# Optimization experiments

Hardware: AMD Instinct MI355X
Metric: run time of the kernel (lower is better)

Reference implementation:

```python
import jax, jax.numpy as jnp
import numpy as np
from jax import lax

DN = ('NCHW', 'OIHW', 'NCHW')


def conv3x3(x, w, b):
    y = lax.conv_general_dilated(x, w, (1, 1), [(1, 1), (1, 1)], dimension_numbers=DN)
    return y + b[None, :, None, None]


def lrelu(x, s):
    return jnp.where(x >= 0, x, s * x)


def layernorm_c(x, g, b, eps=1e-5):
    # LayerNorm over embed_dim; tokens are (h,w), so normalize the channel axis
    m = jnp.mean(x, axis=1, keepdims=True)
    v = jnp.var(x, axis=1, keepdims=True)
    return (x - m) / jnp.sqrt(v + eps) * g[None, :, None, None] + b[None, :, None, None]


def bilateral_corr(x1, x2, md):
    # bilateral cost volume on L2-normalized features:
    # out[b,d,h,w] = <x1n[b,:,h-dy,w-dx], x2n[b,:,h+dy,w+dx]>, (dy,dx) in [-md,md]^2
    def l2n(x):
        return x / jnp.maximum(jnp.linalg.norm(x, axis=1, keepdims=True), 1e-12)
    x1n, x2n = l2n(x1), l2n(x2)
    B, C, H, W = x1.shape
    p1 = jnp.pad(x1n, ((0, 0), (0, 0), (md, md), (md, md)))
    p2 = jnp.pad(x2n, ((0, 0), (0, 0), (md, md), (md, md)))
    outs = []
    for dy in range(-md, md + 1):
        for dx in range(-md, md + 1):
            a = p1[:, :, md - dy:md - dy + H, md - dx:md - dx + W]
            b = p2[:, :, md + dy:md + dy + H, md + dx:md + dx + W]
            outs.append(jnp.sum(a * b, axis=1))
    return jnp.stack(outs, axis=1)  # [B, (2md+1)^2, H, W]


def tail(xt, bi, gln, bln, w0, b0, wr1, br1, wr2, br2, w2, b2, w3, b3, wdec, bdec, wf, bf):
    xt = layernorm_c(xt, gln, bln)
    y = conv3x3(jnp.concatenate([xt, bi], axis=1), w0, b0)
    # resblock(64,64): lrelu(conv2(lrelu(conv1(y))) + y), slope 0.1
    s = y
    r = lrelu(conv3x3(y, wr1, br1), 0.1)
    r = conv3x3(r, wr2, br2) + s
    y = lrelu(r, 0.1)
    y = lrelu(conv3x3(y, w2, b2), 0.2)
    y = lrelu(conv3x3(y, w3, b3), 0.2)
    # ConvTranspose2d(64,64,3,stride=2,pad=1,out_pad=1): lhs-dilated conv with flipped kernel
    wd = jnp.transpose(jnp.flip(wdec, (-2, -1)), (1, 0, 2, 3))  # torch [in,out,kh,kw] -> OIHW
    y = lax.conv_general_dilated(y, wd, (1, 1), [(1, 2), (1, 2)], lhs_dilation=(2, 2), dimension_numbers=DN) + bdec[None, :, None, None]
    flow = conv3x3(y, wf, bf)  # [B, 2, 2H, 2W]
    B, _, H2, W2 = flow.shape
    # F.interpolate(scale_factor=4, mode='bilinear', align_corners=False) * 4
    return jax.image.resize(flow, (B, 2, 4 * H2, 4 * W2), method='bilinear') * 4.0


def setup_inputs():
    key = jax.random.key(0)
    ks = jax.random.split(key, 16)
    B, C, H, W = 4, 256, 96, 160
    md = 3
    r = lambda k, s, sc=0.05: jax.random.normal(k, s, jnp.float32) * sc
    return {
        'x1': jax.random.normal(ks[0], (B, C, H, W), jnp.float32),
        'x2': jax.random.normal(ks[1], (B, C, H, W), jnp.float32),
        'xt': jax.random.normal(ks[2], (B, C, H, W), jnp.float32),
        'gln': jnp.ones((C,), jnp.float32),
        'bln': jnp.zeros((C,), jnp.float32),
        'w0': r(ks[3], (64, C + (2 * md + 1) ** 2, 3, 3)),
        'b0': jnp.zeros((64,), jnp.float32),
        'wr1': r(ks[4], (64, 64, 3, 3)), 'br1': jnp.zeros((64,), jnp.float32),
        'wr2': r(ks[5], (64, 64, 3, 3)), 'br2': jnp.zeros((64,), jnp.float32),
        'w2': r(ks[6], (64, 64, 3, 3)), 'b2': jnp.zeros((64,), jnp.float32),
        'w3': r(ks[7], (64, 64, 3, 3)), 'b3': jnp.zeros((64,), jnp.float32),
        'wdec': r(ks[8], (64, 64, 3, 3)), 'bdec': jnp.zeros((64,), jnp.float32),
        'wf': r(ks[9], (2, 64, 3, 3)), 'bf': jnp.zeros((2,), jnp.float32),
        'corr_range': 3,
    }


def reference(x1, x2, xt, gln, bln, w0, b0, wr1, br1, wr2, br2, w2, b2, w3, b3, wdec, bdec, wf, bf, corr_range):
    bi = bilateral_corr(x1, x2, int(corr_range))
    return tail(xt, bi, gln, bln, w0, b0, wr1, br1, wr2, br2, w2, b2, w3, b3, wdec, bdec, wf, bf)
```

## Files before the change

kernel.cpp:

```cpp
#include <hip/hip_runtime.h>
#include <math.h>

#define HH_ 96
#define WW_ 160
#define HW 15360
#define NPIX 61440
#define CC 256
#define C0 320
#define FF 64
#define H2 192
#define W2 320
#define OHW 61440
#define HO 768
#define WO 1280

typedef __attribute__((ext_vector_type(8))) short short8;
typedef __attribute__((ext_vector_type(4))) float f32x4;

__device__ __forceinline__ float bf2f(ushort u) {
    union { unsigned int i; float f; } v; v.i = ((unsigned int)u) << 16; return v.f;
}
__device__ __forceinline__ ushort f2bf(float f) {
    union { float f; unsigned int i; } v; v.f = f;
    unsigned int u = v.i;
    return (ushort)((u + 0x7FFFu + ((u >> 16) & 1u)) >> 16);
}

__global__ __launch_bounds__(256) void normpack_kernel(
    const float* __restrict__ x1, const float* __restrict__ x2, const float* __restrict__ xt,
    const float* __restrict__ gam, const float* __restrict__ bet,
    ushort* __restrict__ x1c, ushort* __restrict__ x2c,
    ushort* __restrict__ Xhi, float* __restrict__ inv1, float* __restrict__ inv2) {
    __shared__ ushort tile[32 * 258];
    __shared__ float sred[4][32][2];
    const int t = threadIdx.x;
    const int w = t >> 6, l = t & 63;
    const int px4 = l & 7;
    const int cbase = t >> 3;
    const int pxt = blockIdx.x, which = blockIdx.y, b = blockIdx.z;
    const float* src = (which == 0 ? x1 : which == 1 ? x2 : xt);
    src += (size_t)b * CC * HW + pxt * 32;

    float s1[4] = {0.f, 0.f, 0.f, 0.f}, s2[4] = {0.f, 0.f, 0.f, 0.f};
#pragma unroll
    for (int it = 0; it < 8; ++it) {
        int c = it * 32 + cbase;
        f32x4 v4 = *(const f32x4*)(src + (size_t)c * HW + px4 * 4);
#pragma unroll
        for (int j = 0; j < 4; ++j) {
            float f = v4[j];
            s1[j] += f; s2[j] += f * f;
            tile[(px4 * 4 + j) * 258 + c] = f2bf(f);
        }
    }
#pragma unroll
    for (int j = 0; j < 4; ++j) {
        s1[j] += __shfl_xor(s1[j], 8);  s1[j] += __shfl_xor(s1[j], 16); s1[j] += __shfl_xor(s1[j], 32);
        s2[j] += __shfl_xor(s2[j], 8);  s2[j] += __shfl_xor(s2[j], 16); s2[j] += __shfl_xor(s2[j], 32);
    }
    if ((l >> 3) == 0) {
#pragma unroll
        for (int j = 0; j < 4; ++j) {
            sred[w][px4 * 4 + j][0] = s1[j];
            sred[w][px4 * 4 + j][1] = s2[j];
        }
    }
    __syncthreads();

    const int px = t >> 3, grp = t & 7;
    float S1 = sred[0][px][0] + sred[1][px][0] + sred[2][px][0] + sred[3][px][0];
    float S2 = sred[0][px][1] + sred[1][px][1] + sred[2][px][1] + sred[3][px][1];
    const int p = b * HW + pxt * 32 + px;
    const ushort* row = &tile[px * 258];
    if (which < 2) {
        float inv = 1.f / fmaxf(sqrtf(S2), 1e-12f);
        if (grp == 0) (which == 0 ? inv1 : inv2)[p] = inv;
        ushort* dst = (which == 0 ? x1c : x2c) + (size_t)p * CC + grp * 32;
#pragma unroll
        for (int k = 0; k < 4; ++k) {
            short8 o;
#pragma unroll
            for (int h = 0; h < 4; ++h) {
                unsigned int u2 = *(const unsigned int*)(row + grp * 32 + k * 8 + h * 2);
                o[h * 2]     = (short)(u2 & 0xFFFF);
                o[h * 2 + 1] = (short)(u2 >> 16);
            }
            *(short8*)(dst + k * 8) = o;
        }
    } else {
        float m = S1 * (1.f / 256.f);
        float var = fmaxf(S2 * (1.f / 256.f) - m * m, 0.f);
        float rs = rsqrtf(var + 1e-5f);
        ushort* dst = Xhi + (size_t)p * C0 + grp * 32;
#pragma unroll
        for (int k = 0; k < 4; ++k) {
            short8 o;
#pragma unroll
            for (int h = 0; h < 4; ++h) {
                unsigned int u2 = *(const unsigned int*)(row + grp * 32 + k * 8 + h * 2);
                int c = grp * 32 + k * 8 + h * 2;
                float f0 = (bf2f((ushort)(u2 & 0xFFFF)) - m) * rs * gam[c] + bet[c];
                float f1 = (bf2f((ushort)(u2 >> 16)) - m) * rs * gam[c + 1] + bet[c + 1];
                o[h * 2]     = (short)f2bf(f0);
                o[h * 2 + 1] = (short)f2bf(f1);
            }
            *(short8*)(dst + k * 8) = o;
        }
        if (grp < 4) {
            short8 z = {0, 0, 0, 0, 0, 0, 0, 0};
            *(short8*)(Xhi + (size_t)p * C0 + 256 + grp * 16) = z;
            *(short8*)(Xhi + (size_t)p * C0 + 256 + grp * 16 + 8) = z;
        }
    }
}

__global__ __launch_bounds__(256) void corr_mfma_kernel(
    const ushort* __restrict__ x1c, const ushort* __restrict__ x2c,
    const float* __restrict__ inv1, const float* __restrict__ inv2,
    ushort* __restrict__ Xhi) {
    const int lane = threadIdx.x & 63;
    const int wv = threadIdx.x >> 6;
    const int sid = ((blockIdx.x & 7) * 120) + (blockIdx.x >> 3);
    const int b  = sid / 240;
    const int rem = sid % 240;
    const int uq = rem / 10, xt = rem % 10;
    const int u = uq * 4 + wv;
    const int x0 = xt * 16;
    const int jl = lane & 15;
    const int kg = lane >> 4;
    const short8 zero8 = {0, 0, 0, 0, 0, 0, 0, 0};

    short8 qf[8];
    {
        size_t qb = ((size_t)b * HW + u * WW_ + x0 + jl) * CC + kg * 8;
#pragma unroll
        for (int ks = 0; ks < 8; ++ks)
            qf[ks] = *(const short8*)(x1c + qb + ks * 32);
    }
    float iv1v[4];
#pragma unroll
    for (int r = 0; r < 4; ++r)
        iv1v[r] = inv1[b * HW + u * WW_ + x0 + kg * 4 + r];

    for (int dy = -3; dy <= 3; ++dy) {
        const int y = u + dy;
        if ((unsigned)y >= (unsigned)HH_) continue;
        const int w = u + 2 * dy;
        const bool rowok = (unsigned)w < (unsigned)HH_;

        f32x4 acc0 = (f32x4){0.f, 0.f, 0.f, 0.f};
        f32x4 acc1 = (f32x4){0.f, 0.f, 0.f, 0.f};
        if (rowok) {
#pragma unroll
            for (int nt = 0; nt < 2; ++nt) {
                int kx = x0 - 6 + jl + 16 * nt;
                bool ok = (unsigned)kx < (unsigned)WW_;
                int kxc = min(max(kx, 0), WW_ - 1);
                size_t kb = ((size_t)b * HW + w * WW_ + kxc) * CC + kg * 8;
#pragma unroll
                for (int ks = 0; ks < 8; ++ks) {
                    short8 bv = *(const short8*)(x2c + kb + ks * 32);
                    if (!ok) bv = zero8;
                    if (nt == 0)
                        acc0 = __builtin_amdgcn_mfma_f32_16x16x32_bf16(qf[ks], bv, acc0, 0, 0, 0);
                    else
                        acc1 = __builtin_amdgcn_mfma_f32_16x16x32_bf16(qf[ks], bv, acc1, 0, 0, 0);
                }
            }
        }
#pragma unroll
        for (int nt = 0; nt < 2; ++nt) {
            int j = jl + 16 * nt;
#pragma unroll
            for (int r = 0; r < 4; ++r) {
                int q = kg * 4 + r;
                int tt = j - q - 6;
                if (tt & 1) continue;
                int dx = tt >> 1;
                if (dx < -3 || dx > 3) continue;
                int cx = x0 + q + dx;
                if ((unsigned)cx >= (unsigned)WW_) continue;
                float v = 0.f;
                if (rowok) {
                    int pbx = min(max(x0 + q + 2 * dx, 0), WW_ - 1);
                    float iv2 = inv2[b * HW + w * WW_ + pbx];
                    v = (nt == 0 ? acc0[r] : acc1[r]) * iv1v[r] * iv2;
                }
                size_t o = ((size_t)(b * HW + y * WW_ + cx)) * C0
                         + 256 + (dy + 3) * 7 + (dx + 3);
                Xhi[o] = f2bf(v);
            }
        }
    }
}

__global__ void pack_w_all(const float* __restrict__ w0, const float* __restrict__ wr1,
                           const float* __restrict__ wr2, const float* __restrict__ w2,
                           const float* __restrict__ w3, const float* __restrict__ wdec,
                           ushort* __restrict__ W0, ushort* __restrict__ WR1,
                           ushort* __restrict__ WR2, ushort* __restrict__ W2o,
                           ushort* __restrict__ W3o, ushort* __restrict__ WD) {
    int job = blockIdx.y;
    const float* w = job == 0 ? w0 : job == 1 ? wr1 : job == 2 ? wr2
                   : job == 3 ? w2 : job == 4 ? w3 : wdec;
    ushort* dst = job == 0 ? W0 : job == 1 ? WR1 : job == 2 ? WR2
                : job == 3 ? W2o : job == 4 ? W3o : WD;
    int CinReal = job == 0 ? 305 : 64;
    int KC = job == 0 ? 10 : 2;
    int isDeconv = (job == 5);
    int gid = blockIdx.x * blockDim.x + threadIdx.x;
    int total = 9 * KC * 4 * 64;
    if (gid >= total) return;
    int lane = gid & 63;
    int nt = (gid >> 6) & 3;
    int kc = (gid >> 8) % KC;
    int slot = (gid >> 8) / KC;
    int co = nt * 16 + (lane & 15);
    int ky = slot / 3, kx = slot % 3;
    for (int j = 0; j < 8; ++j) {
        int ci = kc * 32 + (lane >> 4) * 8 + j;
        float v = 0.f;
        if (ci < CinReal) {
            if (isDeconv) v = w[((size_t)(ci * 64 + co) * 3 + (2 - ky)) * 3 + (2 - kx)];
            else          v = w[((size_t)(co * CinReal + ci) * 3 + ky) * 3 + kx];
        }
        dst[(size_t)gid * 8 + j] = f2bf(v);
    }
}

template<int KC>
__global__ __launch_bounds__(256, 4) void conv_lds_t(
    const ushort* __restrict__ Ahi,
    const ushort* __restrict__ Whi,
    const float* __restrict__ bias,
    ushort* __restrict__ Ohi,
    const ushort* __restrict__ Rhi,
    float slope, int act, int hasres) {
    constexpr int CIN = KC * 32;
    __shared__ ushort lds[2 * 3488];
    const int t = threadIdx.x;
    const int lane = t & 63;
    const int wave = t >> 6;
    const int kg = lane >> 4;
    const int jl = lane & 15;
    const short8 zero8 = {0, 0, 0, 0, 0, 0, 0, 0};

    const int sid = ((blockIdx.x & 7) * 120) + (blockIdx.x >> 3);
    const int b0 = sid / 240;
    const int rm = sid % 240;
    const int yq = rm / 10, xw = rm % 10;
    const int y0 = yq * 4;
    const int x0 = xw * 16;
    const size_t rowbase = (size_t)b0 * HW;

    f32x4 acc[4];
#pragma unroll
    for (int nt = 0; nt < 4; ++nt) acc[nt] = (f32x4){0.f, 0.f, 0.f, 0.f};

    auto stage = [&](ushort* buf, int kc) {
#pragma unroll
        for (int i = 0; i < 2; ++i) {
            int e = t + i * 256;
            if (e < 432) {
                int kge = e & 3;
                int q = e >> 2;
                int pe = q % 18;
                int re = q / 18;
                int gy = y0 - 1 + re, gx = x0 - 1 + pe;
                bool ok = ((unsigned)gy < 96u) && ((unsigned)gx < 160u);
                short8 vh = zero8;
                if (ok) {
                    size_t ga = ((rowbase + gy * WW_ + gx) * (size_t)CIN) + kc * 32 + kge * 8;
                    vh = *(const short8*)(Ahi + ga);
                }
                *(short8*)(buf + kge * 872 + (re * 18 + pe) * 8) = vh;
            }
        }
    };

    stage(lds, 0);

#pragma unroll 1
    for (int kc = 0; kc < KC; ++kc) {
        __syncthreads();
        if (kc + 1 < KC) stage(lds + ((kc + 1) & 1) * 3488, kc + 1);
        const ushort* bufc = lds + (kc & 1) * 3488;
#pragma unroll
        for (int tap = 0; tap < 9; ++tap) {
            const int dy = tap / 3 - 1, dx = tap % 3 - 1;
            const int abase = kg * 872 + (wave + dy + 1) * 144 + (jl + dx + 1) * 8;
            short8 ah = *(const short8*)(bufc + abase);
            const ushort* wt = Whi + (size_t)(tap * KC + kc) * 2048;
#pragma unroll
            for (int nt = 0; nt < 4; ++nt) {
                short8 bh = *(const short8*)(wt + (nt * 64 + lane) * 8);
                acc[nt] = __builtin_amdgcn_mfma_f32_16x16x32_bf16(ah, bh, acc[nt], 0, 0, 0);
            }
        }
    }

#pragma unroll
    for (int r = 0; r < 4; ++r) {
        size_t pr = rowbase + (y0 + wave) * WW_ + x0 + kg * 4 + r;
#pragma unroll
        for (int nt = 0; nt < 4; ++nt) {
            int co = nt * 16 + jl;
            float vv = acc[nt][r] + bias[co];
            size_t oo = pr * 64 + co;
            if (hasres) vv += bf2f(Rhi[oo]);
            if (act) vv = vv >= 0.f ? vv : vv * slope;
            Ohi[oo] = f2bf(vv);
        }
    }
}

__global__ __launch_bounds__(256, 8) void conv_lds2(
    const ushort* __restrict__ Ahi,
    const ushort* __restrict__ Whi,
    const float* __restrict__ bias,
    ushort* __restrict__ Ohi,
    const ushort* __restrict__ Rhi,
    float slope, int act, int hasres) {
    __shared__ ushort lds[2 * 2336];
    const int t = threadIdx.x;
    const int lane = t & 63;
    const int wave = t >> 6;
    const int row_w = wave >> 1;
    const int coh = wave & 1;
    const int kg = lane >> 4;
    const int jl = lane & 15;
    const short8 zero8 = {0, 0, 0, 0, 0, 0, 0, 0};

    const int sid = ((blockIdx.x & 7) * 240) + (blockIdx.x >> 3);
    const int b0 = sid / 480;
    const int rm = sid % 480;
    const int yp = rm / 10, xw = rm % 10;
    const int y0 = yp * 2;
    const int x0 = xw * 16;
    const size_t rowbase = (size_t)b0 * HW;

    f32x4 acc[2];
    acc[0] = (f32x4){0.f, 0.f, 0.f, 0.f};
    acc[1] = (f32x4){0.f, 0.f, 0.f, 0.f};

    auto stage = [&](ushort* buf, int kc) {
#pragma unroll
        for (int i = 0; i < 2; ++i) {
            int e = t + i * 256;
            if (e < 288) {
                int kge = e & 3;
                int q = e >> 2;
                int pe = q % 18;
                int re = q / 18;
                int gy = y0 - 1 + re, gx = x0 - 1 + pe;
                bool ok = ((unsigned)gy < 96u) && ((unsigned)gx < 160u);
                short8 vh = zero8;
                if (ok) {
                    size_t ga = ((rowbase + gy * WW_ + gx) * 64) + kc * 32 + kge * 8;
                    vh = *(const short8*)(Ahi + ga);
                }
                *(short8*)(buf + kge * 584 + (re * 18 + pe) * 8) = vh;
            }
        }
    };

    stage(lds, 0);

#pragma unroll 1
    for (int kc = 0; kc < 2; ++kc) {
        __syncthreads();
        if (kc == 0) stage(lds + 2336, 1);
        const ushort* bufc = lds + (kc & 1) * 2336;
#pragma unroll
        for (int tap = 0; tap < 9; ++tap) {
            const int dy = tap / 3 - 1, dx = tap % 3 - 1;
            const int abase = kg * 584 + (row_w + dy + 1) * 144 + (jl + dx + 1) * 8;
            short8 ah = *(const short8*)(bufc + abase);
            const ushort* wt = Whi + (size_t)(tap * 2 + kc) * 2048;
#pragma unroll
            for (int nt = 0; nt < 2; ++nt) {
                short8 bh = *(const short8*)(wt + (((coh << 1) | nt) * 64 + lane) * 8);
                acc[nt] = __builtin_amdgcn_mfma_f32_16x16x32_bf16(ah, bh, acc[nt], 0, 0, 0);
            }
        }
    }

#pragma unroll
    for (int r = 0; r < 4; ++r) {
        size_t pr = rowbase + (y0 + row_w) * WW_ + x0 + kg * 4 + r;
#pragma unroll
        for (int nt = 0; nt < 2; ++nt) {
            int co = ((coh << 1) | nt) * 16 + jl;
            float vv = acc[nt][r] + bias[co];
            size_t oo = pr * 64 + co;
            if (hasres) vv += bf2f(Rhi[oo]);
            if (act) vv = vv >= 0.f ? vv : vv * slope;
            Ohi[oo] = f2bf(vv);
        }
    }
}

__global__ __launch_bounds__(256, 6) void deconv_fused_kernel(
    const ushort* __restrict__ Ahi,
    const ushort* __restrict__ Whi,
    const float* __restrict__ bias,
    ushort* __restrict__ decb) {
    const int lane = threadIdx.x & 63;
    const int wave = threadIdx.x >> 6;
    const int row_w = wave >> 1;
    const int coh = wave & 1;
    const int kg = lane >> 4;
    const short8 zero8 = {0, 0, 0, 0, 0, 0, 0, 0};

    const int sid = ((blockIdx.x & 7) * 240) + (blockIdx.x >> 3);
    const int b0 = sid / 480;
    const int rm = sid % 480;
    const int yp = rm / 10, xh = rm % 10;
    const int y0 = yp * 2 + row_w;
    const int x0 = xh * 16;
    const size_t rowbase = (size_t)b0 * HW;

    f32x4 acc[4][2];
#pragma unroll
    for (int p = 0; p < 4; ++p) {
        acc[p][0] = (f32x4){0.f, 0.f, 0.f, 0.f};
        acc[p][1] = (f32x4){0.f, 0.f, 0.f, 0.f};
    }

    const int nuse[4]   = {4, 2, 2, 1};
    const int upar[4][4] = {{0, 1, 2, 3}, {1, 3, -1, -1}, {2, 3, -1, -1}, {3, -1, -1, -1}};
    const int uslt[4][4] = {{4, 3, 1, 0}, {5, 2, -1, -1}, {7, 6, -1, -1}, {8, -1, -1, -1}};

#pragma unroll
    for (int o = 0; o < 4; ++o) {
        const int ody = o >> 1, odx = o & 1;
        int yy = y0 + ody, xx = x0 + (lane & 15) + odx;
        bool v = (unsigned)yy < 96u && (unsigned)xx < 160u;
        int yyc = min(yy, 95), xxc = min(xx, 159);
        size_t a = (rowbase + yyc * WW_ + xxc) * 64 + kg * 8;
#pragma unroll
        for (int kc = 0; kc < 2; ++kc) {
            short8 ah = *(const short8*)(Ahi + a + kc * 32);
            if (!v) ah = zero8;
#pragma unroll
            for (int u = 0; u < 4; ++u) {
                if (u >= nuse[o]) break;
                int par = upar[o][u], slot = uslt[o][u];
#pragma unroll
                for (int nt = 0; nt < 2; ++nt) {
                    short8 bh = *(const short8*)(Whi + ((size_t)slot * 2 + kc) * 2048
                                                 + (((coh << 1) | nt) * 64 + lane) * 8);
                    acc[par][nt] = __builtin_amdgcn_mfma_f32_16x16x32_bf16(ah, bh, acc[par][nt], 0, 0, 0);
                }
            }
        }
    }

#pragma unroll
    for (int r = 0; r < 4; ++r) {
        int x2 = x0 + kg * 4 + r;
#pragma unroll
        for (int par = 0; par < 4; ++par) {
            int py = par >> 1, px = par & 1;
            size_t po = ((size_t)b0 * H2 + 2 * y0 + py) * W2 + 2 * x2 + px;
#pragma unroll
            for (int nt = 0; nt < 2; ++nt) {
                int co = ((coh << 1) | nt) * 16 + (lane & 15);
                decb[po * 64 + co] = f2bf(acc[par][nt][r] + bias[co]);
            }
        }
    }
}

__global__ __launch_bounds__(256) void flow_kernel(const ushort* __restrict__ decb,
                                                   const float* __restrict__ wf,
                                                   const float* __restrict__ bf2v,
                                                   float* __restrict__ flow) {
    __shared__ float wsm[1152];
    for (int i = threadIdx.x; i < 1152; i += 256) wsm[i] = wf[i];
    __syncthreads();
    int fid = ((blockIdx.x & 7) * 240) + (blockIdx.x >> 3);
    int tid = fid * 256 + threadIdx.x;
    int p = tid >> 1, half = tid & 1;
    if (p >= 4 * OHW) return;
    int b = p / OHW, rem = p % OHW, oy = rem / W2, ox = rem % W2;
    float a0 = 0.f, a1 = 0.f;
    for (int ky = 0; ky < 3; ++ky) {
        int yy = oy + ky - 1;
        if ((unsigned)yy >= (unsigned)H2) continue;
        for (int kx = 0; kx < 3; ++kx) {
            int xx = ox + kx - 1;
            if ((unsigned)xx >= (unsigned)W2) continue;
            size_t base = ((size_t)b * OHW + yy * W2 + xx) * 64;
            int tap = ky * 3 + kx;
#pragma unroll
            for (int c8 = 0; c8 < 4; ++c8) {
                int cg = half * 4 + c8;
                short8 v8 = *(const short8*)(decb + base + cg * 8);
#pragma unroll
                for (int j = 0; j < 8; ++j) {
                    float f = bf2f((ushort)v8[j]);
                    int ci = cg * 8 + j;
                    a0 += f * wsm[ci * 9 + tap];
                    a1 += f * wsm[(64 + ci) * 9 + tap];
                }
            }
        }
    }
    a0 += __shfl_xor(a0, 1);
    a1 += __shfl_xor(a1, 1);
    if (half == 0) {
        flow[(size_t)(b * 2 + 0) * OHW + rem] = a0 + bf2v[0];
        flow[(size_t)(b * 2 + 1) * OHW + rem] = a1 + bf2v[1];
    }
}

__global__ __launch_bounds__(256) void resize_kernel(const float* __restrict__ flow,
                                                     float* __restrict__ out) {
    int idx = blockIdx.x * blockDim.x + threadIdx.x;
    int total = 4 * 2 * HO * (WO / 4);
    if (idx >= total) return;
    int qx = idx % (WO / 4);
    int oy = (idx / (WO / 4)) % HO;
    int c  = (idx / ((WO / 4) * HO)) % 2;
    int b  = idx / ((WO / 4) * HO * 2);

    float sy = (oy + 0.5f) * 0.25f - 0.5f;
    int y0 = (int)floorf(sy);
    float fy = sy - y0;
    int y0c = min(max(y0, 0), H2 - 1);
    int y1c = min(max(y0 + 1, 0), H2 - 1);
    const float* r0 = flow + ((size_t)(b * 2 + c) * H2 + y0c) * W2;
    const float* r1 = flow + ((size_t)(b * 2 + c) * H2 + y1c) * W2;
    int xm = max(qx - 1, 0), xp = min(qx + 1, W2 - 1);
    float fm = (1.f - fy) * r0[xm] + fy * r1[xm];
    float f0 = (1.f - fy) * r0[qx] + fy * r1[qx];
    float fp = (1.f - fy) * r0[xp] + fy * r1[xp];
    f32x4 o;
    o[0] = (0.375f * fm + 0.625f * f0) * 4.0f;
    o[1] = (0.125f * fm + 0.875f * f0) * 4.0f;
    o[2] = (0.875f * f0 + 0.125f * fp) * 4.0f;
    o[3] = (0.625f * f0 + 0.375f * fp) * 4.0f;
    *(f32x4*)(out + (((size_t)(b * 2 + c) * HO + oy) * WO) + qx * 4) = o;
}

extern "C" void kernel_launch(void* const* d_in, const int* in_sizes, int n_in,
                              void* d_out, int out_size, void* d_ws, size_t ws_size,
                              hipStream_t stream) {
    const float* x1   = (const float*)d_in[0];
    const float* x2   = (const float*)d_in[1];
    const float* xt   = (const float*)d_in[2];
    const float* gln  = (const float*)d_in[3];
    const float* bln  = (const float*)d_in[4];
    const float* w0   = (const float*)d_in[5];
    const float* b0   = (const float*)d_in[6];
    const float* wr1  = (const float*)d_in[7];
    const float* br1  = (const float*)d_in[8];
    const float* wr2  = (const float*)d_in[9];
    const float* br2  = (const float*)d_in[10];
    const float* w2   = (const float*)d_in[11];
    const float* b2   = (const float*)d_in[12];
    const float* w3   = (const float*)d_in[13];
    const float* b3   = (const float*)d_in[14];
    const float* wdec = (const float*)d_in[15];
    const float* bdec = (const float*)d_in[16];
    const float* wf   = (const float*)d_in[17];
    const float* bfv  = (const float*)d_in[18];
    float* out = (float*)d_out;

    char* ws = (char*)d_ws;
    ushort* x1c  = (ushort*)(ws + 0);
    ushort* x2c  = (ushort*)(ws + 31457280);
    ushort* X0hi = (ushort*)(ws + 62914560);
    ushort* y0hi = (ushort*)(ws + 102236160);
    ushort* t1hi = (ushort*)(ws + 110100480);
    ushort* t2hi = (ushort*)(ws + 117964800);
    ushort* decb = (ushort*)(ws + 0);
    float*  flowb = (float*)(ws + 62914560);
    char* wp = ws + 125829120;
    ushort* W0hi  = (ushort*)(wp);
    ushort* WR1hi = (ushort*)(wp + 368640);
    ushort* WR2hi = (ushort*)(wp + 442368);
    ushort* W2hi  = (ushort*)(wp + 516096);
    ushort* W3hi  = (ushort*)(wp + 589824);
    ushort* WDhi  = (ushort*)(wp + 663552);
    float*  inv1  = (float*)(wp + 786432);
    float*  inv2  = (float*)(wp + 1048576);

    pack_w_all<<<dim3(90, 6), 256, 0, stream>>>(w0, wr1, wr2, w2, w3, wdec,
        W0hi, WR1hi, WR2hi, W2hi, W3hi, WDhi);

    normpack_kernel<<<dim3(480, 3, 4), 256, 0, stream>>>(
        x1, x2, xt, gln, bln, x1c, x2c, X0hi, inv1, inv2);
    corr_mfma_kernel<<<960, 256, 0, stream>>>(x1c, x2c, inv1, inv2, X0hi);

    conv_lds_t<10><<<960, 256, 0, stream>>>(X0hi, W0hi, b0, y0hi, nullptr, 0.f, 0, 0);
    conv_lds2<<<1920, 256, 0, stream>>>(y0hi, WR1hi, br1, t1hi, nullptr, 0.1f, 1, 0);
    conv_lds2<<<1920, 256, 0, stream>>>(t1hi, WR2hi, br2, t2hi, y0hi, 0.1f, 1, 1);
    conv_lds2<<<1920, 256, 0, stream>>>(t2hi, W2hi, b2, t1hi, nullptr, 0.2f, 1, 0);
    conv_lds2<<<1920, 256, 0, stream>>>(t1hi, W3hi, b3, t2hi, nullptr, 0.2f, 1, 0);
    deconv_fused_kernel<<<1920, 256, 0, stream>>>(t2hi, WDhi, bdec, decb);

    flow_kernel<<<1920, 256, 0, stream>>>(decb, wf, bfv, flowb);
    resize_kernel<<<7680, 256, 0, stream>>>(flowb, out);

    (void)in_sizes; (void)n_in; (void)out_size; (void)ws_size;
}
```

Measured before the change: 336.6 us.

## Retile first conv to 8-row tiles with 512 threads and split output channels

```diff
diff --git a/kernel.cpp b/kernel.cpp
--- a/kernel.cpp
+++ b/kernel.cpp
@@ -228,40 +228,42 @@
     }
 }
 
-template<int KC>
-__global__ __launch_bounds__(256, 4) void conv_lds_t(
+__global__ __launch_bounds__(512) void conv0_kernel(
     const ushort* __restrict__ Ahi,
     const ushort* __restrict__ Whi,
     const float* __restrict__ bias,
-    ushort* __restrict__ Ohi,
-    const ushort* __restrict__ Rhi,
-    float slope, int act, int hasres) {
-    constexpr int CIN = KC * 32;
-    __shared__ ushort lds[2 * 3488];
+    ushort* __restrict__ Ohi) {
+    constexpr int KC = 10, CIN = 320;
+    __shared__ ushort lds[2 * 5920];
     const int t = threadIdx.x;
     const int lane = t & 63;
     const int wave = t >> 6;
+    const int rp = wave >> 1;
+    const int coh = wave & 1;
     const int kg = lane >> 4;
     const int jl = lane & 15;
     const short8 zero8 = {0, 0, 0, 0, 0, 0, 0, 0};
 
-    const int sid = ((blockIdx.x & 7) * 120) + (blockIdx.x >> 3);
-    const int b0 = sid / 240;
-    const int rm = sid % 240;
-    const int yq = rm / 10, xw = rm % 10;
-    const int y0 = yq * 4;
+    const int sid = ((blockIdx.x & 7) * 60) + (blockIdx.x >> 3);
+    const int b0 = sid / 120;
+    const int rm = sid % 120;
+    const int yo = rm / 10, xw = rm % 10;
+    const int y0 = yo * 8;
     const int x0 = xw * 16;
     const size_t rowbase = (size_t)b0 * HW;
 
-    f32x4 acc[4];
-#pragma unroll
-    for (int nt = 0; nt < 4; ++nt) acc[nt] = (f32x4){0.f, 0.f, 0.f, 0.f};
+    f32x4 acc[2][2];
+#pragma unroll
+    for (int r = 0; r < 2; ++r) {
+        acc[r][0] = (f32x4){0.f, 0.f, 0.f, 0.f};
+        acc[r][1] = (f32x4){0.f, 0.f, 0.f, 0.f};
+    }
 
     auto stage = [&](ushort* buf, int kc) {
 #pragma unroll
         for (int i = 0; i < 2; ++i) {
-            int e = t + i * 256;
-            if (e < 432) {
+            int e = t + i * 512;
+            if (e < 720) {
                 int kge = e & 3;
                 int q = e >> 2;
                 int pe = q % 18;
@@ -273,7 +275,7 @@
                     size_t ga = ((rowbase + gy * WW_ + gx) * (size_t)CIN) + kc * 32 + kge * 8;
                     vh = *(const short8*)(Ahi + ga);
                 }
-                *(short8*)(buf + kge * 872 + (re * 18 + pe) * 8) = vh;
+                *(short8*)(buf + kge * 1480 + (re * 18 + pe) * 8) = vh;
             }
         }
     };
@@ -283,33 +285,35 @@
 #pragma unroll 1
     for (int kc = 0; kc < KC; ++kc) {
         __syncthreads();
-        if (kc + 1 < KC) stage(lds + ((kc + 1) & 1) * 3488, kc + 1);
-        const ushort* bufc = lds + (kc & 1) * 3488;
+        if (kc + 1 < KC) stage(lds + ((kc + 1) & 1) * 5920, kc + 1);
+        const ushort* bufc = lds + (kc & 1) * 5920;
 #pragma unroll
         for (int tap = 0; tap < 9; ++tap) {
             const int dy = tap / 3 - 1, dx = tap % 3 - 1;
-            const int abase = kg * 872 + (wave + dy + 1) * 144 + (jl + dx + 1) * 8;
-            short8 ah = *(const short8*)(bufc + abase);
+            const int a0i = kg * 1480 + ((rp * 2 + 0 + dy + 1) * 18 + (jl + dx + 1)) * 8;
+            const int a1i = kg * 1480 + ((rp * 2 + 1 + dy + 1) * 18 + (jl + dx + 1)) * 8;
+            short8 ah0 = *(const short8*)(bufc + a0i);
+            short8 ah1 = *(const short8*)(bufc + a1i);
             const ushort* wt = Whi + (size_t)(tap * KC + kc) * 2048;
 #pragma unroll
-            for (int nt = 0; nt < 4; ++nt) {
-                short8 bh = *(const short8*)(wt + (nt * 64 + lane) * 8);
-                acc[nt] = __builtin_amdgcn_mfma_f32_16x16x32_bf16(ah, bh, acc[nt], 0, 0, 0);
-            }
-        }
-    }
-
-#pragma unroll
-    for (int r = 0; r < 4; ++r) {
-        size_t pr = rowbase + (y0 + wave) * WW_ + x0 + kg * 4 + r;
-#pragma unroll
-        for (int nt = 0; nt < 4; ++nt) {
-            int co = nt * 16 + jl;
-            float vv = acc[nt][r] + bias[co];
-            size_t oo = pr * 64 + co;
-            if (hasres) vv += bf2f(Rhi[oo]);
-            if (act) vv = vv >= 0.f ? vv : vv * slope;
-            Ohi[oo] = f2bf(vv);
+            for (int nt = 0; nt < 2; ++nt) {
+                short8 bh = *(const short8*)(wt + (((coh << 1) | nt) * 64 + lane) * 8);
+                acc[0][nt] = __builtin_amdgcn_mfma_f32_16x16x32_bf16(ah0, bh, acc[0][nt], 0, 0, 0);
+                acc[1][nt] = __builtin_amdgcn_mfma_f32_16x16x32_bf16(ah1, bh, acc[1][nt], 0, 0, 0);
+            }
+        }
+    }
+
+#pragma unroll
+    for (int rr = 0; rr < 2; ++rr) {
+#pragma unroll
+        for (int r = 0; r < 4; ++r) {
+            size_t pr = rowbase + (y0 + rp * 2 + rr) * WW_ + x0 + kg * 4 + r;
+#pragma unroll
+            for (int nt = 0; nt < 2; ++nt) {
+                int co = ((coh << 1) | nt) * 16 + jl;
+                Ohi[pr * 64 + co] = f2bf(acc[rr][nt][r] + bias[co]);
+            }
         }
     }
 }
@@ -594,7 +598,7 @@
         x1, x2, xt, gln, bln, x1c, x2c, X0hi, inv1, inv2);
     corr_mfma_kernel<<<960, 256, 0, stream>>>(x1c, x2c, inv1, inv2, X0hi);
 
-    conv_lds_t<10><<<960, 256, 0, stream>>>(X0hi, W0hi, b0, y0hi, nullptr, 0.f, 0, 0);
+    conv0_kernel<<<480, 512, 0, stream>>>(X0hi, W0hi, b0, y0hi);
     conv_lds2<<<1920, 256, 0, stream>>>(y0hi, WR1hi, br1, t1hi, nullptr, 0.1f, 1, 0);
     conv_lds2<<<1920, 256, 0, stream>>>(t1hi, WR2hi, br2, t2hi, y0hi, 0.1f, 1, 1);
     conv_lds2<<<1920, 256, 0, stream>>>(t2hi, W2hi, b2, t1hi, nullptr, 0.2f, 1, 0);
```

After: 321.4 us, median of 2. -4.5%, faster.
